# Performance work log

Hardware: AMD Instinct MI355X
Metric: run time of the kernel (lower is better)

The kernel has to match this reference:

```python
import jax, jax.numpy as jnp
import numpy as np

B, C, H, W = 8, 256, 64, 64
RED = 16

def setup_inputs() -> dict:
    key = jax.random.key(0)
    ks = jax.random.split(key, 10)
    s = 0.05
    return {
        "x": jax.random.normal(ks[0], (B, C, H, W), jnp.float32),
        "ca_w1": jax.random.normal(ks[1], (C // RED, C), jnp.float32) * s,
        "ca_w2": jax.random.normal(ks[2], (C, C // RED), jnp.float32) * s,
        "q_w": jax.random.normal(ks[3], (C // RED, C), jnp.float32) * s,
        "q_b": jax.random.normal(ks[4], (C // RED,), jnp.float32) * s,
        "k_w": jax.random.normal(ks[5], (C // RED, C), jnp.float32) * s,
        "k_b": jax.random.normal(ks[6], (C // RED,), jnp.float32) * s,
        "v_w": jax.random.normal(ks[7], (C, C), jnp.float32) * s,
        "v_b": jax.random.normal(ks[8], (C,), jnp.float32) * s,
        "gamma": jax.random.normal(ks[9], (1,), jnp.float32) * s,
    }

def _cbam(x, ca_w1, ca_w2, q_w, q_b, k_w, k_b, v_w, v_b, gamma):
    # ---- Channel attention (squeeze-excite with avg+max pooling) ----
    avg = jnp.mean(x, axis=(2, 3))          # [B, C]
    mx = jnp.max(x, axis=(2, 3))            # [B, C]
    def fc(s):
        h = jax.nn.relu(jnp.einsum('rc,bc->br', ca_w1, s))
        return jnp.einsum('cr,br->bc', ca_w2, h)
    gate = jax.nn.sigmoid(fc(avg) + fc(mx))[:, :, None, None]
    x = x * gate
    # ---- Spatial (non-local) attention ----
    b, c, h, w = x.shape
    hw = h * w
    xf = x.reshape(b, c, hw)                          # [B, C, HW]
    q = jnp.einsum('rc,bcn->brn', q_w, xf) + q_b[None, :, None]   # [B, C/r, HW]
    k = jnp.einsum('rc,bcn->brn', k_w, xf) + k_b[None, :, None]
    v = jnp.einsum('oc,bcn->bon', v_w, xf) + v_b[None, :, None]   # [B, C, HW]
    attn = jax.nn.softmax(jnp.einsum('bri,brj->bij', q, k), axis=-1)  # [B, HW, HW]
    out = jnp.einsum('bcj,bij->bci', v, attn).reshape(b, c, h, w)
    return gamma[0] * out + x

def reference(x, ca_w1, ca_w2, q_w, q_b, k_w, k_b, v_w, v_b, gamma):
    return _cbam(x, ca_w1, ca_w2, q_w, q_b, k_w, k_b, v_w, v_b, gamma)
```

## Files before the change

### kernel.cpp

```cpp
#include <hip/hip_runtime.h>
#include <hip/hip_bf16.h>
#include <math.h>

#define BB 8
#define CCH 256
#define HWN 4096
#define RR 16

typedef __attribute__((ext_vector_type(8))) short short8;
typedef __attribute__((ext_vector_type(4))) float f32x4;

static __device__ __forceinline__ unsigned short f2bf(float x) {
    union { float f; unsigned u; } v; v.f = x;
    return (unsigned short)((v.u + 0x8000u) >> 16);
}

__global__ __launch_bounds__(256) void k_pool(const float* __restrict__ x,
                                              float* __restrict__ avgp,
                                              float* __restrict__ maxp,
                                              const float* __restrict__ vw,
                                              const float* __restrict__ qw,
                                              const float* __restrict__ kw,
                                              unsigned short* __restrict__ Wb) {
    int bc = blockIdx.x;
    int t = threadIdx.x;
    if (bc < 288) {
        int idx = bc * 256 + t;
        int m = idx >> 8, c = idx & 255;
        float v;
        if (m < 256) v = vw[idx];
        else if (m < 272) v = qw[(m - 256) * 256 + c];
        else v = kw[(m - 272) * 256 + c];
        Wb[idx] = f2bf(v);
    }
    const float4* p = (const float4*)(x + (size_t)bc * HWN);
    float s = 0.f, m = -INFINITY;
#pragma unroll
    for (int i = 0; i < 4; ++i) {
        float4 v = p[t + 256 * i];
        s += v.x + v.y + v.z + v.w;
        m = fmaxf(m, fmaxf(fmaxf(v.x, v.y), fmaxf(v.z, v.w)));
    }
    for (int off = 32; off; off >>= 1) {
        s += __shfl_down(s, off);
        m = fmaxf(m, __shfl_down(m, off));
    }
    __shared__ float ss[4], sm[4];
    int wid = t >> 6;
    if ((t & 63) == 0) { ss[wid] = s; sm[wid] = m; }
    __syncthreads();
    if (t == 0) {
        float S = ss[0] + ss[1] + ss[2] + ss[3];
        float M = fmaxf(fmaxf(sm[0], sm[1]), fmaxf(sm[2], sm[3]));
        avgp[bc] = S * (1.f / (float)HWN);
        maxp[bc] = M;
    }
}

__global__ __launch_bounds__(512, 2) void k_proj(const float* __restrict__ x,
                                                 const float* __restrict__ avgp,
                                                 const float* __restrict__ maxp,
                                                 const float* __restrict__ w1,
                                                 const float* __restrict__ w2,
                                                 const unsigned short* __restrict__ Wb,
                                                 const float* __restrict__ vb,
                                                 const float* __restrict__ qb,
                                                 const float* __restrict__ kb,
                                                 float* __restrict__ gate,
                                                 unsigned short* __restrict__ qT,
                                                 unsigned short* __restrict__ kT,
                                                 unsigned short* __restrict__ vB) {
    int b = blockIdx.x & 7;
    int n0 = (blockIdx.x >> 3) << 6;
    int t = threadIdx.x;
    int w = t >> 6, l = t & 63, quad = l >> 4, ln = l & 15;
    int mh = w >> 2;
    int ws = w & 3;

    __shared__ __align__(16) unsigned short xs_t[64][72];
    __shared__ __align__(16) unsigned short vtile[256 * 72];
    __shared__ float qk_s[32][66];
    __shared__ float sa[CCH], sx[CCH], sh[32], gs[CCH];

    const f32x4 zf = {0.f, 0.f, 0.f, 0.f};
    f32x4 acc[9];
#pragma unroll
    for (int a = 0; a < 9; ++a) acc[a] = zf;

    if (t < CCH) {
        sa[t] = avgp[b * CCH + t];
        sx[t] = maxp[b * CCH + t];
    }

    const float* xp[2];
#pragma unroll
    for (int it = 0; it < 2; ++it) {
        int idx = it * 512 + t;
        int cl = idx >> 4, nq = idx & 15;
        xp[it] = x + (((size_t)(b * CCH + cl)) << 12) + n0 + nq * 4;
    }
    float4 xr[2];
#pragma unroll
    for (int it = 0; it < 2; ++it) xr[it] = *(const float4*)xp[it];

    __syncthreads();
    if (t < 32) {
        int r = t & 15;
        const float* src = (t < 16) ? sa : sx;
        float h = 0.f;
        for (int c = 0; c < CCH; ++c) h += w1[r * CCH + c] * src[c];
        sh[t] = fmaxf(h, 0.f);
    }
    __syncthreads();
    if (t < CCH) {
        float g = 0.f;
#pragma unroll
        for (int r = 0; r < RR; ++r) g += w2[t * RR + r] * (sh[r] + sh[16 + r]);
        float gv = 1.f / (1.f + __expf(-g));
        gs[t] = gv;
        if (n0 == 0) gate[b * CCH + t] = gv;
    }

    for (int cc = 0; cc < 4; ++cc) {
        __syncthreads();
#pragma unroll
        for (int it = 0; it < 2; ++it) {
            int idx = it * 512 + t;
            int cl = idx >> 4, nq = idx & 15;
            int c = cc * 64 + cl;
            float g = gs[c];
            float4 v = xr[it];
            xs_t[nq * 4 + 0][cl] = f2bf(v.x * g);
            xs_t[nq * 4 + 1][cl] = f2bf(v.y * g);
            xs_t[nq * 4 + 2][cl] = f2bf(v.z * g);
            xs_t[nq * 4 + 3][cl] = f2bf(v.w * g);
        }
        __syncthreads();

        if (cc < 3) {
#pragma unroll
            for (int it = 0; it < 2; ++it)
                xr[it] = *(const float4*)(xp[it] + (((size_t)(cc + 1)) << 18));
        }

        short8 bfrag[2];
#pragma unroll
        for (int kc = 0; kc < 2; ++kc)
            bfrag[kc] = *(const short8*)&xs_t[ws * 16 + ln][kc * 32 + quad * 8];

#pragma unroll
        for (int mtl = 0; mtl < 8; ++mtl) {
#pragma unroll
            for (int kc = 0; kc < 2; ++kc) {
                short8 af = *(const short8*)(Wb + ((size_t)(mh * 128 + mtl * 16 + ln)) * 256 + cc * 64 + kc * 32 + quad * 8);
                acc[mtl] = __builtin_amdgcn_mfma_f32_16x16x32_bf16(af, bfrag[kc], acc[mtl], 0, 0, 0);
            }
        }
#pragma unroll
        for (int kc = 0; kc < 2; ++kc) {
            short8 af = *(const short8*)(Wb + ((size_t)(256 + mh * 16 + ln)) * 256 + cc * 64 + kc * 32 + quad * 8);
            acc[8] = __builtin_amdgcn_mfma_f32_16x16x32_bf16(af, bfrag[kc], acc[8], 0, 0, 0);
        }
    }

#pragma unroll
    for (int mtl = 0; mtl < 8; ++mtl) {
#pragma unroll
        for (int r = 0; r < 4; ++r) {
            int m = mh * 128 + mtl * 16 + quad * 4 + r;
            vtile[m * 72 + ws * 16 + ln] = f2bf(acc[mtl][r] + vb[m]);
        }
    }
#pragma unroll
    for (int r = 0; r < 4; ++r)
        qk_s[mh * 16 + quad * 4 + r][ws * 16 + ln] = acc[8][r];
    __syncthreads();

    {
        unsigned short* vBp = vB + (((size_t)b) << 20);
        int c = t & 255, Qh = (t >> 8) * 4;
#pragma unroll
        for (int qq = 0; qq < 4; ++qq) {
            int Q = Qh + qq;
            short8 v8 = *(const short8*)(vtile + c * 72 + Q * 8);
            *(short8*)(vBp + ((size_t)((((n0 >> 3) + Q) << 8) + c) << 3)) = v8;
        }
    }
    if (t < 128) {
        int isK = t >> 6;
        int n = t & 63;
        const float* bias = isK ? kb : qb;
        unsigned u32[8];
#pragma unroll
        for (int j = 0; j < 8; ++j) {
            unsigned lo = f2bf(qk_s[isK * 16 + 2 * j][n] + bias[2 * j]);
            unsigned hi = f2bf(qk_s[isK * 16 + 2 * j + 1][n] + bias[2 * j + 1]);
            u32[j] = lo | (hi << 16);
        }
        unsigned short* dst = (isK ? kT : qT) + ((size_t)(b * HWN + n0 + n)) * RR;
        uint4 d0 = {u32[0], u32[1], u32[2], u32[3]};
        uint4 d1 = {u32[4], u32[5], u32[6], u32[7]};
        ((uint4*)dst)[0] = d0;
        ((uint4*)dst)[1] = d1;
    }
}

__global__ __launch_bounds__(512, 4) void k_attn(const unsigned short* __restrict__ qT,
                                                 const unsigned short* __restrict__ kT,
                                                 const unsigned short* __restrict__ vB,
                                                 const float* __restrict__ x,
                                                 const float* __restrict__ gate,
                                                 const float* __restrict__ gamma,
                                                 float* __restrict__ out) {
    int b = blockIdx.x & 7;
    int i0 = (blockIdx.x >> 3) << 6;
    int t = threadIdx.x;
    int w = __builtin_amdgcn_readfirstlane(t >> 6);
    int l = t & 63;
    int quad = l >> 4, ln = l & 15;
    int jsub = w >> 1;
    int ih = w & 1;
    int c0 = w * 32;

    __shared__ __align__(16) unsigned short p_lds[4][4096];
    __shared__ float l_s[4][68];

    const short8 zs = {0, 0, 0, 0, 0, 0, 0, 0};
    const f32x4 zf = {0.f, 0.f, 0.f, 0.f};

    short8 bq[2];
    bq[0] = zs; bq[1] = zs;
    if (quad < 2) {
#pragma unroll
        for (int u = 0; u < 2; ++u)
            bq[u] = *(const short8*)(qT + (((size_t)(b * HWN + i0 + ih * 32 + u * 16 + ln)) << 4) + (quad << 3));
    }

    f32x4 acc[2][4];
#pragma unroll
    for (int cs = 0; cs < 2; ++cs)
#pragma unroll
        for (int is = 0; is < 4; ++is) acc[cs][is] = zf;
    float lsum[2] = {0.f, 0.f};

    const float c1 = 1.44269504f;
    const float c0e = -11.5415603f;

    const unsigned short* kb_u = kT + ((size_t)(b * HWN)) * RR;
    const int kln = ((jsub * 16 + ln) << 4) + (quad << 3);
    const unsigned short* vb_u = vB + (((size_t)b) << 20) + ((size_t)c0 << 3);
    int vln[4];
#pragma unroll
    for (int ks = 0; ks < 2; ++ks)
#pragma unroll
        for (int cs = 0; cs < 2; ++cs)
            vln[ks * 2 + cs] = (((ks * 4 + quad) << 8) + cs * 16 + ln) << 3;

    int soff = ((jsub * 2 + (quad >> 1)) * 64 + ih * 32 + ln) * 8 + (quad & 1) * 4;
    int rbase = quad * 512 + ln * 8;

    short8 akA = zs, akB = zs;
    short8 avA[4], avB[4];

    auto load_ak = [&](short8& ak, int j0) {
        if (quad < 2) ak = *(const short8*)(kb_u + ((j0 << 4) + kln));
    };
    auto load_av = [&](short8 (&av)[4], int j0) {
        const unsigned short* vp = vb_u + (j0 << 8);
#pragma unroll
        for (int u = 0; u < 4; ++u) av[u] = *(const short8*)(vp + vln[u]);
    };

    load_ak(akA, 0);
    load_ak(akB, 64);
    load_av(avA, 0);
    load_av(avB, 64);

    auto finish_s = [&](const f32x4& sf, unsigned short* pbuf, int u) {
        float p0 = exp2f(fmaf(sf[0], c1, c0e));
        float p1 = exp2f(fmaf(sf[1], c1, c0e));
        float p2 = exp2f(fmaf(sf[2], c1, c0e));
        float p3 = exp2f(fmaf(sf[3], c1, c0e));
        lsum[u] += (p0 + p1) + (p2 + p3);
        uint2 pk;
        asm("v_cvt_pk_bf16_f32 %0, %1, %2" : "=v"(pk.x) : "v"(p0), "v"(p1));
        asm("v_cvt_pk_bf16_f32 %0, %1, %2" : "=v"(pk.y) : "v"(p2), "v"(p3));
        *(uint2*)(pbuf + soff + u * 128) = pk;
    };

    auto pv = [&](const short8 (&av)[4], const unsigned short* pbuf) {
#pragma unroll
        for (int ks = 0; ks < 2; ++ks) {
            short8 bp[4];
#pragma unroll
            for (int is = 0; is < 4; ++is)
                bp[is] = *(const short8*)(pbuf + rbase + ks * 2048 + is * 128);
#pragma unroll
            for (int cs = 0; cs < 2; ++cs)
#pragma unroll
                for (int is = 0; is < 4; ++is)
                    acc[cs][is] = __builtin_amdgcn_mfma_f32_16x16x32_bf16(av[ks * 2 + cs], bp[is], acc[cs][is], 0, 0, 0);
        }
    };

    for (int jt = 0; jt < 32; ++jt) {
        unsigned short* pb0 = &p_lds[(jt & 1) * 2 + 0][0];
        unsigned short* pb1 = &p_lds[(jt & 1) * 2 + 1][0];

        f32x4 sf00 = __builtin_amdgcn_mfma_f32_16x16x32_bf16(akA, bq[0], zf, 0, 0, 0);
        f32x4 sf01 = __builtin_amdgcn_mfma_f32_16x16x32_bf16(akA, bq[1], zf, 0, 0, 0);
        f32x4 sf10 = __builtin_amdgcn_mfma_f32_16x16x32_bf16(akB, bq[0], zf, 0, 0, 0);
        f32x4 sf11 = __builtin_amdgcn_mfma_f32_16x16x32_bf16(akB, bq[1], zf, 0, 0, 0);
        finish_s(sf00, pb0, 0);
        finish_s(sf01, pb0, 1);
        finish_s(sf10, pb1, 0);
        finish_s(sf11, pb1, 1);

        __syncthreads();

        bool pf = jt < 31;
        int j0n = (jt + 1) << 7;
        if (pf) { load_ak(akA, j0n); load_ak(akB, j0n + 64); }

        pv(avA, pb0);
        if (pf) load_av(avA, j0n);
        pv(avB, pb1);
        if (pf) load_av(avB, j0n + 64);
    }

    lsum[0] += __shfl_xor(lsum[0], 16, 64);
    lsum[0] += __shfl_xor(lsum[0], 32, 64);
    lsum[1] += __shfl_xor(lsum[1], 16, 64);
    lsum[1] += __shfl_xor(lsum[1], 32, 64);
    if (l < 16) {
        l_s[jsub][ih * 32 + l] = lsum[0];
        l_s[jsub][ih * 32 + 16 + l] = lsum[1];
    }
    __syncthreads();

    float g = gamma[0];
    float rinv[4];
#pragma unroll
    for (int is = 0; is < 4; ++is) {
        int i = is * 16 + ln;
        float lf = (l_s[0][i] + l_s[1][i]) + (l_s[2][i] + l_s[3][i]);
        rinv[is] = g / lf;
    }

#pragma unroll
    for (int cs = 0; cs < 2; ++cs) {
#pragma unroll
        for (int r = 0; r < 4; ++r) {
            int c = c0 + cs * 16 + quad * 4 + r;
            float gc = gate[b * CCH + c];
            size_t rowoff = (((size_t)(b * CCH + c)) << 12) + i0;
            float* po = out + rowoff;
            const float* px = x + rowoff;
#pragma unroll
            for (int is = 0; is < 4; ++is) {
                int idx = is * 16 + ln;
                po[idx] = acc[cs][is][r] * rinv[is] + px[idx] * gc;
            }
        }
    }
}

extern "C" void kernel_launch(void* const* d_in, const int* in_sizes, int n_in,
                              void* d_out, int out_size, void* d_ws, size_t ws_size,
                              hipStream_t stream) {
    const float* x = (const float*)d_in[0];
    const float* w1 = (const float*)d_in[1];
    const float* w2 = (const float*)d_in[2];
    const float* qw = (const float*)d_in[3];
    const float* qb = (const float*)d_in[4];
    const float* kw = (const float*)d_in[5];
    const float* kb = (const float*)d_in[6];
    const float* vw = (const float*)d_in[7];
    const float* vb = (const float*)d_in[8];
    const float* gamma = (const float*)d_in[9];
    float* out = (float*)d_out;
    char* ws = (char*)d_ws;

    float* avgp = (float*)(ws);
    float* maxp = (float*)(ws + 8192);
    float* gate = (float*)(ws + 16384);
    unsigned short* Wb = (unsigned short*)(ws + 24576);
    unsigned short* qT = (unsigned short*)(ws + 24576 + 147456);
    unsigned short* kT = (unsigned short*)(ws + 24576 + 147456 + 1048576);
    unsigned short* vB = (unsigned short*)(ws + 24576 + 147456 + 2097152);

    k_pool<<<2048, 256, 0, stream>>>(x, avgp, maxp, vw, qw, kw, Wb);
    k_proj<<<512, 512, 0, stream>>>(x, avgp, maxp, w1, w2, Wb, vb, qb, kb, gate, qT, kT, vB);
    k_attn<<<512, 512, 0, stream>>>(qT, kT, vB, x, gate, gamma, out);
}
```

Measured before the change: 221.7 us.

## Split attention blocks by channel half, 4 waves each computing all 64 query rows

The attention kernel now launches 1024 blocks of 256 threads. Each block handles half of the output channels, and each wave computes scores for all 64 query rows of one key sub-tile instead of half of them. This gives more, smaller blocks, but the QK^T scores and softmax exponentials are recomputed in both channel-half blocks, doubling that work. Each block still uses the same LDS footprint, so occupancy may be limited by LDS rather than thread count.

```diff
diff --git a/kernel.cpp b/kernel.cpp
--- a/kernel.cpp
+++ b/kernel.cpp
@@ -205,7 +205,7 @@
     }
 }
 
-__global__ __launch_bounds__(512, 4) void k_attn(const unsigned short* __restrict__ qT,
+__global__ __launch_bounds__(256, 4) void k_attn(const unsigned short* __restrict__ qT,
                                                  const unsigned short* __restrict__ kT,
                                                  const unsigned short* __restrict__ vB,
                                                  const float* __restrict__ x,
@@ -213,14 +213,14 @@
                                                  const float* __restrict__ gamma,
                                                  float* __restrict__ out) {
     int b = blockIdx.x & 7;
-    int i0 = (blockIdx.x >> 3) << 6;
+    int ch = (blockIdx.x >> 3) & 1;
+    int i0 = (blockIdx.x >> 4) << 6;
     int t = threadIdx.x;
     int w = __builtin_amdgcn_readfirstlane(t >> 6);
     int l = t & 63;
     int quad = l >> 4, ln = l & 15;
-    int jsub = w >> 1;
-    int ih = w & 1;
-    int c0 = w * 32;
+    int jsub = w;
+    int c0 = ch * 128 + w * 32;
 
     __shared__ __align__(16) unsigned short p_lds[4][4096];
     __shared__ float l_s[4][68];
@@ -228,12 +228,13 @@
     const short8 zs = {0, 0, 0, 0, 0, 0, 0, 0};
     const f32x4 zf = {0.f, 0.f, 0.f, 0.f};
 
-    short8 bq[2];
-    bq[0] = zs; bq[1] = zs;
+    short8 bq[4];
+#pragma unroll
+    for (int u = 0; u < 4; ++u) bq[u] = zs;
     if (quad < 2) {
 #pragma unroll
-        for (int u = 0; u < 2; ++u)
-            bq[u] = *(const short8*)(qT + (((size_t)(b * HWN + i0 + ih * 32 + u * 16 + ln)) << 4) + (quad << 3));
+        for (int u = 0; u < 4; ++u)
+            bq[u] = *(const short8*)(qT + (((size_t)(b * HWN + i0 + u * 16 + ln)) << 4) + (quad << 3));
     }
 
     f32x4 acc[2][4];
@@ -241,7 +242,7 @@
     for (int cs = 0; cs < 2; ++cs)
 #pragma unroll
         for (int is = 0; is < 4; ++is) acc[cs][is] = zf;
-    float lsum[2] = {0.f, 0.f};
+    float lsum[4] = {0.f, 0.f, 0.f, 0.f};
 
     const float c1 = 1.44269504f;
     const float c0e = -11.5415603f;
@@ -256,7 +257,7 @@
         for (int cs = 0; cs < 2; ++cs)
             vln[ks * 2 + cs] = (((ks * 4 + quad) << 8) + cs * 16 + ln) << 3;
 
-    int soff = ((jsub * 2 + (quad >> 1)) * 64 + ih * 32 + ln) * 8 + (quad & 1) * 4;
+    int soff = ((jsub * 2 + (quad >> 1)) * 64 + ln) * 8 + (quad & 1) * 4;
     int rbase = quad * 512 + ln * 8;
 
     short8 akA = zs, akB = zs;
@@ -307,14 +308,17 @@
         unsigned short* pb0 = &p_lds[(jt & 1) * 2 + 0][0];
         unsigned short* pb1 = &p_lds[(jt & 1) * 2 + 1][0];
 
-        f32x4 sf00 = __builtin_amdgcn_mfma_f32_16x16x32_bf16(akA, bq[0], zf, 0, 0, 0);
-        f32x4 sf01 = __builtin_amdgcn_mfma_f32_16x16x32_bf16(akA, bq[1], zf, 0, 0, 0);
-        f32x4 sf10 = __builtin_amdgcn_mfma_f32_16x16x32_bf16(akB, bq[0], zf, 0, 0, 0);
-        f32x4 sf11 = __builtin_amdgcn_mfma_f32_16x16x32_bf16(akB, bq[1], zf, 0, 0, 0);
-        finish_s(sf00, pb0, 0);
-        finish_s(sf01, pb0, 1);
-        finish_s(sf10, pb1, 0);
-        finish_s(sf11, pb1, 1);
+        f32x4 sA[4], sB[4];
+#pragma unroll
+        for (int u = 0; u < 4; ++u)
+            sA[u] = __builtin_amdgcn_mfma_f32_16x16x32_bf16(akA, bq[u], zf, 0, 0, 0);
+#pragma unroll
+        for (int u = 0; u < 4; ++u)
+            sB[u] = __builtin_amdgcn_mfma_f32_16x16x32_bf16(akB, bq[u], zf, 0, 0, 0);
+#pragma unroll
+        for (int u = 0; u < 4; ++u) finish_s(sA[u], pb0, u);
+#pragma unroll
+        for (int u = 0; u < 4; ++u) finish_s(sB[u], pb1, u);
 
         __syncthreads();
 
@@ -328,13 +332,15 @@
         if (pf) load_av(avB, j0n + 64);
     }
 
-    lsum[0] += __shfl_xor(lsum[0], 16, 64);
-    lsum[0] += __shfl_xor(lsum[0], 32, 64);
-    lsum[1] += __shfl_xor(lsum[1], 16, 64);
-    lsum[1] += __shfl_xor(lsum[1], 32, 64);
+#pragma unroll
+    for (int u = 0; u < 4; ++u) {
+        lsum[u] += __shfl_xor(lsum[u], 16, 64);
+        lsum[u] += __shfl_xor(lsum[u], 32, 64);
+    }
     if (l < 16) {
-        l_s[jsub][ih * 32 + l] = lsum[0];
-        l_s[jsub][ih * 32 + 16 + l] = lsum[1];
+#pragma unroll
+        for (int u = 0; u < 4; ++u)
+            l_s[jsub][u * 16 + l] = lsum[u];
     }
     __syncthreads();
 
@@ -391,5 +397,5 @@
 
     k_pool<<<2048, 256, 0, stream>>>(x, avgp, maxp, vw, qw, kw, Wb);
     k_proj<<<512, 512, 0, stream>>>(x, avgp, maxp, w1, w2, Wb, vb, qb, kb, gate, qT, kT, vB);
-    k_attn<<<512, 512, 0, stream>>>(qT, kT, vB, x, gate, gamma, out);
+    k_attn<<<1024, 256, 0, stream>>>(qT, kT, vB, x, gate, gamma, out);
 }
```

Result: slower. 279.4 us (+26.0%).
